# Kernel optimization log

Hardware: AMD Instinct MI355X
Metric: run time of the kernel (lower is better)

The kernel has to match this reference:

```python
import jax, jax.numpy as jnp
import numpy as np

N_NODES = 100000
N_EDGES = 1600000
NODE_IN = 64   # == node_out (residual)
EDGE_OUT = 48
HID = 128
N_GRAPHS = 64
MLP_IN = NODE_IN + 3 * EDGE_OUT + 1  # 209


def setup_inputs() -> dict:
    key = jax.random.key(0)
    ks = jax.random.split(key, 9)
    x = jax.random.normal(ks[0], (N_NODES, NODE_IN), dtype=jnp.float32)
    edge_index = jax.random.randint(ks[1], (2, N_EDGES), 0, N_NODES, dtype=jnp.int64)
    edge_attr = jax.random.normal(ks[2], (N_EDGES, EDGE_OUT), dtype=jnp.float32)
    u = jax.random.normal(ks[3], (N_GRAPHS, 1), dtype=jnp.float32)
    batch = jnp.sort(jax.random.randint(ks[4], (N_NODES,), 0, N_GRAPHS, dtype=jnp.int64))
    # MLP params (Linear stores weight [out,in]; we keep [in,out] for x @ W)
    W1 = jax.random.normal(ks[5], (MLP_IN, HID), dtype=jnp.float32) / np.sqrt(MLP_IN)
    b1 = jnp.zeros((HID,), dtype=jnp.float32)
    W2 = jax.random.normal(ks[6], (HID, NODE_IN), dtype=jnp.float32) / np.sqrt(HID)
    b2 = jnp.zeros((NODE_IN,), dtype=jnp.float32)
    return {"x": x, "edge_index": edge_index, "edge_attr": edge_attr, "u": u,
            "batch": batch, "W1": W1, "b1": b1, "W2": W2, "b2": b2}


def reference(x, edge_index, edge_attr, u, batch, W1, b1, W2, b2):
    col = edge_index[1]                      # destination node per edge
    n = x.shape[0]
    # sum / count / max over edges grouped by destination node
    s = jax.ops.segment_sum(edge_attr, col, num_segments=n)           # [N, E_out]
    cnt = jax.ops.segment_sum(jnp.ones((edge_attr.shape[0], 1), edge_attr.dtype),
                              col, num_segments=n)                    # [N, 1]
    m = jax.ops.segment_max(edge_attr, col, num_segments=n)           # [N, E_out]
    m = jnp.where(cnt > 0, m, jnp.zeros((), edge_attr.dtype))         # empty -> 0 (torch_scatter)
    mean = s / jnp.maximum(cnt, 1.0)                                  # empty -> 0
    h = jnp.concatenate([x, s, m, mean, u[batch]], axis=1)            # [N, MLP_IN]
    h = jax.nn.relu(h @ W1 + b1)
    out = h @ W2 + b2
    return out + x  # residual
```

## Files before the change

### kernel.cpp

```cpp
#include <hip/hip_runtime.h>

#define N_NODES 100000
#define N_EDGES 1600000
#define NODE_IN 64
#define EDGE_OUT 48
#define HID 128
#define MLP_IN 209
#define NB 32

__global__ void init_ws(float* __restrict__ s, float* __restrict__ m,
                        float* __restrict__ cnt) {
    int i = blockIdx.x * 256 + threadIdx.x;
    int tot = N_NODES * EDGE_OUT;
    if (i < tot) {
        s[i] = 0.0f;
        ((int*)m)[i] = 0xff800000;
    }
    if (i < N_NODES) cnt[i] = 0.0f;
}

__device__ __forceinline__ void atomicMaxF(float* addr, float val) {
    if (val >= 0.0f) {
        atomicMax((int*)addr, __float_as_int(val));
    } else {
        atomicMin((unsigned int*)addr, __float_as_uint(val));
    }
}

__global__ __launch_bounds__(256) void scatter_edges(
        const float* __restrict__ ea, const int* __restrict__ col,
        float* __restrict__ s, float* __restrict__ m, float* __restrict__ cnt) {
    int i = blockIdx.x * 256 + threadIdx.x;
    if (i >= N_EDGES * EDGE_OUT) return;
    int e = i / EDGE_OUT;
    int f = i - e * EDGE_OUT;
    float v = ea[i];
    int d = col[e];
    atomicAdd(&s[d * EDGE_OUT + f], v);
    atomicMaxF(&m[d * EDGE_OUT + f], v);
    if (f == 0) atomicAdd(&cnt[d], 1.0f);
}

__global__ __launch_bounds__(256) void mlp_kernel(
        const float* __restrict__ x, const float* __restrict__ u,
        const int* __restrict__ batch,
        const float* __restrict__ W1, const float* __restrict__ b1,
        const float* __restrict__ W2, const float* __restrict__ b2,
        const float* __restrict__ s, const float* __restrict__ m,
        const float* __restrict__ cnt, float* __restrict__ out) {
    __shared__ float h[NB][MLP_IN + 3];
    __shared__ float h1[NB][HID + 2];
    const int t = threadIdx.x;
    const int node0 = blockIdx.x * NB;

    for (int i = t; i < NB * MLP_IN; i += 256) {
        int r = i / MLP_IN;
        int c = i - r * MLP_IN;
        int g = node0 + r;
        float v;
        if (c < 64) {
            v = x[g * 64 + c];
        } else if (c < 112) {
            v = s[g * 48 + (c - 64)];
        } else if (c < 160) {
            float mv = m[g * 48 + (c - 112)];
            v = (cnt[g] > 0.0f) ? mv : 0.0f;
        } else if (c < 208) {
            v = s[g * 48 + (c - 160)] / fmaxf(cnt[g], 1.0f);
        } else {
            v = u[batch[g]];
        }
        h[r][c] = v;
    }
    __syncthreads();

    {
        const int j0 = (t & 31) * 4;
        const int r0 = (t >> 5) * 4;
        float acc[4][4];
        #pragma unroll
        for (int a = 0; a < 4; a++)
            #pragma unroll
            for (int b = 0; b < 4; b++) acc[a][b] = b1[j0 + b];
        for (int k = 0; k < MLP_IN; k++) {
            float4 w = *(const float4*)&W1[k * HID + j0];
            float hv[4];
            #pragma unroll
            for (int a = 0; a < 4; a++) hv[a] = h[r0 + a][k];
            #pragma unroll
            for (int a = 0; a < 4; a++) {
                acc[a][0] += hv[a] * w.x;
                acc[a][1] += hv[a] * w.y;
                acc[a][2] += hv[a] * w.z;
                acc[a][3] += hv[a] * w.w;
            }
        }
        #pragma unroll
        for (int a = 0; a < 4; a++)
            #pragma unroll
            for (int b = 0; b < 4; b++)
                h1[r0 + a][j0 + b] = fmaxf(acc[a][b], 0.0f);
    }
    __syncthreads();

    {
        const int j0 = (t & 15) * 4;
        const int r0 = (t >> 4) * 2;
        float acc[2][4];
        #pragma unroll
        for (int a = 0; a < 2; a++)
            #pragma unroll
            for (int b = 0; b < 4; b++) acc[a][b] = b2[j0 + b];
        for (int k = 0; k < HID; k++) {
            float4 w = *(const float4*)&W2[k * NODE_IN + j0];
            #pragma unroll
            for (int a = 0; a < 2; a++) {
                float hv = h1[r0 + a][k];
                acc[a][0] += hv * w.x;
                acc[a][1] += hv * w.y;
                acc[a][2] += hv * w.z;
                acc[a][3] += hv * w.w;
            }
        }
        #pragma unroll
        for (int a = 0; a < 2; a++) {
            int g = node0 + r0 + a;
            float4 o;
            o.x = acc[a][0] + h[r0 + a][j0 + 0];
            o.y = acc[a][1] + h[r0 + a][j0 + 1];
            o.z = acc[a][2] + h[r0 + a][j0 + 2];
            o.w = acc[a][3] + h[r0 + a][j0 + 3];
            *(float4*)&out[g * NODE_IN + j0] = o;
        }
    }
}

extern "C" void kernel_launch(void* const* d_in, const int* in_sizes, int n_in,
                              void* d_out, int out_size, void* d_ws, size_t ws_size,
                              hipStream_t stream) {
    const float* x     = (const float*)d_in[0];
    const int*   ei    = (const int*)d_in[1];
    const float* ea    = (const float*)d_in[2];
    const float* u     = (const float*)d_in[3];
    const int*   batch = (const int*)d_in[4];
    const float* W1    = (const float*)d_in[5];
    const float* b1    = (const float*)d_in[6];
    const float* W2    = (const float*)d_in[7];
    const float* b2    = (const float*)d_in[8];
    float* out = (float*)d_out;

    float* s   = (float*)d_ws;
    float* m   = s + (size_t)N_NODES * EDGE_OUT;
    float* cnt = m + (size_t)N_NODES * EDGE_OUT;

    const int* col = ei + N_EDGES;

    int initTot = N_NODES * EDGE_OUT;
    hipLaunchKernelGGL(init_ws, dim3((initTot + 255) / 256), dim3(256), 0, stream,
                       s, m, cnt);

    int scTot = N_EDGES * EDGE_OUT;
    hipLaunchKernelGGL(scatter_edges, dim3((scTot + 255) / 256), dim3(256), 0, stream,
                       ea, col, s, m, cnt);

    hipLaunchKernelGGL(mlp_kernel, dim3(N_NODES / NB), dim3(256), 0, stream,
                       x, u, batch, W1, b1, W2, b2, s, m, cnt, out);
}
```

Measured before the change: 1.315 ms.

## Replace atomic edge scatter with CSR build and fused per-node gather-reduce in MLP

Instead of scattering every edge feature with float atomicAdd and atomicMax into node-sized buffers, the edges are bucketed by destination into a CSR index (count, single-block scan, fill). The MLP kernel then gathers each node's incoming edge rows, reduces sum and max with wave shuffles, and writes the aggregates straight into a transposed shared tile. This removes about 150M atomics and the round trip of the s and m buffers through memory. In exchange it does random row gathers through eix, runs a serial single-block scan, and transposes the shared layout so the first matmul can use vectorized loads.

```diff
diff --git a/kernel.cpp b/kernel.cpp
--- a/kernel.cpp
+++ b/kernel.cpp
@@ -1,4 +1,5 @@
 #include <hip/hip_runtime.h>
+#include <math.h>
 
 #define N_NODES 100000
 #define N_EDGES 1600000
@@ -7,70 +8,122 @@
 #define HID 128
 #define MLP_IN 209
 #define NB 32
-
-__global__ void init_ws(float* __restrict__ s, float* __restrict__ m,
-                        float* __restrict__ cnt) {
+#define HTS 36
+#define H1S 132
+
+__global__ void k_zero(int* __restrict__ cur) {
     int i = blockIdx.x * 256 + threadIdx.x;
-    int tot = N_NODES * EDGE_OUT;
-    if (i < tot) {
-        s[i] = 0.0f;
-        ((int*)m)[i] = 0xff800000;
-    }
-    if (i < N_NODES) cnt[i] = 0.0f;
-}
-
-__device__ __forceinline__ void atomicMaxF(float* addr, float val) {
-    if (val >= 0.0f) {
-        atomicMax((int*)addr, __float_as_int(val));
-    } else {
-        atomicMin((unsigned int*)addr, __float_as_uint(val));
-    }
-}
-
-__global__ __launch_bounds__(256) void scatter_edges(
-        const float* __restrict__ ea, const int* __restrict__ col,
-        float* __restrict__ s, float* __restrict__ m, float* __restrict__ cnt) {
-    int i = blockIdx.x * 256 + threadIdx.x;
-    if (i >= N_EDGES * EDGE_OUT) return;
-    int e = i / EDGE_OUT;
-    int f = i - e * EDGE_OUT;
-    float v = ea[i];
-    int d = col[e];
-    atomicAdd(&s[d * EDGE_OUT + f], v);
-    atomicMaxF(&m[d * EDGE_OUT + f], v);
-    if (f == 0) atomicAdd(&cnt[d], 1.0f);
-}
-
-__global__ __launch_bounds__(256) void mlp_kernel(
-        const float* __restrict__ x, const float* __restrict__ u,
-        const int* __restrict__ batch,
+    if (i < N_NODES) cur[i] = 0;
+}
+
+__global__ __launch_bounds__(256) void k_count(const int* __restrict__ col,
+                                               int* __restrict__ cur) {
+    int e = blockIdx.x * 256 + threadIdx.x;
+    if (e < N_EDGES) atomicAdd(&cur[col[e]], 1);
+}
+
+__global__ __launch_bounds__(1024) void k_scan(int* __restrict__ cur,
+                                               int* __restrict__ off) {
+    __shared__ int part[1024];
+    const int t = threadIdx.x;
+    const int CH = (N_NODES + 1023) / 1024;
+    const int base = t * CH;
+    int sum = 0;
+    for (int i = 0; i < CH; i++) {
+        int idx = base + i;
+        if (idx < N_NODES) sum += cur[idx];
+    }
+    part[t] = sum;
+    __syncthreads();
+    for (int o = 1; o < 1024; o <<= 1) {
+        int v = 0;
+        if (t >= o) v = part[t - o];
+        __syncthreads();
+        part[t] += v;
+        __syncthreads();
+    }
+    int run = part[t] - sum;
+    for (int i = 0; i < CH; i++) {
+        int idx = base + i;
+        if (idx < N_NODES) {
+            int d = cur[idx];
+            off[idx] = run;
+            cur[idx] = run;
+            run += d;
+        }
+    }
+    if (t == 1023) off[N_NODES] = run;
+}
+
+__global__ __launch_bounds__(256) void k_fill(const int* __restrict__ col,
+                                              int* __restrict__ cur,
+                                              int* __restrict__ eix) {
+    int e = blockIdx.x * 256 + threadIdx.x;
+    if (e < N_EDGES) {
+        int pos = atomicAdd(&cur[col[e]], 1);
+        eix[pos] = e;
+    }
+}
+
+__global__ __launch_bounds__(256) void k_mlp(
+        const float* __restrict__ x, const float* __restrict__ ea,
+        const float* __restrict__ u, const int* __restrict__ batch,
         const float* __restrict__ W1, const float* __restrict__ b1,
         const float* __restrict__ W2, const float* __restrict__ b2,
-        const float* __restrict__ s, const float* __restrict__ m,
-        const float* __restrict__ cnt, float* __restrict__ out) {
-    __shared__ float h[NB][MLP_IN + 3];
-    __shared__ float h1[NB][HID + 2];
+        const int* __restrict__ off, const int* __restrict__ eix,
+        float* __restrict__ out) {
+    __shared__ float ht[MLP_IN * HTS];
+    __shared__ float h1[NB * H1S];
     const int t = threadIdx.x;
     const int node0 = blockIdx.x * NB;
 
-    for (int i = t; i < NB * MLP_IN; i += 256) {
-        int r = i / MLP_IN;
-        int c = i - r * MLP_IN;
-        int g = node0 + r;
-        float v;
-        if (c < 64) {
-            v = x[g * 64 + c];
-        } else if (c < 112) {
-            v = s[g * 48 + (c - 64)];
-        } else if (c < 160) {
-            float mv = m[g * 48 + (c - 112)];
-            v = (cnt[g] > 0.0f) ? mv : 0.0f;
-        } else if (c < 208) {
-            v = s[g * 48 + (c - 160)] / fmaxf(cnt[g], 1.0f);
-        } else {
-            v = u[batch[g]];
-        }
-        h[r][c] = v;
+    for (int i = t; i < NB * NODE_IN; i += 256) {
+        int r = i >> 6, c = i & 63;
+        ht[c * HTS + r] = x[(node0 + r) * NODE_IN + c];
+    }
+    if (t < NB) ht[208 * HTS + t] = u[batch[node0 + t]];
+
+    {
+        const int wv = t >> 6;
+        const int lane = t & 63;
+        const int f = lane & 15;
+        const int g = lane >> 4;
+        for (int i = 0; i < 8; i++) {
+            const int r = wv * 8 + i;
+            const int n = node0 + r;
+            const int beg = off[n], end = off[n + 1];
+            float s0 = 0.f, s1 = 0.f, s2 = 0.f;
+            float m0 = -INFINITY, m1 = -INFINITY, m2 = -INFINITY;
+            for (int p = beg + g; p < end; p += 4) {
+                const int e = eix[p];
+                const float* row = ea + (size_t)e * EDGE_OUT;
+                float v0 = row[f];
+                float v1 = row[f + 16];
+                float v2 = row[f + 32];
+                s0 += v0; s1 += v1; s2 += v2;
+                m0 = fmaxf(m0, v0); m1 = fmaxf(m1, v1); m2 = fmaxf(m2, v2);
+            }
+            #pragma unroll
+            for (int d = 16; d < 64; d <<= 1) {
+                s0 += __shfl_xor(s0, d); s1 += __shfl_xor(s1, d); s2 += __shfl_xor(s2, d);
+                m0 = fmaxf(m0, __shfl_xor(m0, d));
+                m1 = fmaxf(m1, __shfl_xor(m1, d));
+                m2 = fmaxf(m2, __shfl_xor(m2, d));
+            }
+            const int deg = end - beg;
+            if (lane < 16) {
+                const float fd = fmaxf((float)deg, 1.0f);
+                ht[(64 + f) * HTS + r] = s0;
+                ht[(64 + f + 16) * HTS + r] = s1;
+                ht[(64 + f + 32) * HTS + r] = s2;
+                ht[(112 + f) * HTS + r] = (deg > 0) ? m0 : 0.f;
+                ht[(112 + f + 16) * HTS + r] = (deg > 0) ? m1 : 0.f;
+                ht[(112 + f + 32) * HTS + r] = (deg > 0) ? m2 : 0.f;
+                ht[(160 + f) * HTS + r] = s0 / fd;
+                ht[(160 + f + 16) * HTS + r] = s1 / fd;
+                ht[(160 + f + 32) * HTS + r] = s2 / fd;
+            }
+        }
     }
     __syncthreads();
 
@@ -82,24 +135,20 @@
         for (int a = 0; a < 4; a++)
             #pragma unroll
             for (int b = 0; b < 4; b++) acc[a][b] = b1[j0 + b];
+        #pragma unroll 4
         for (int k = 0; k < MLP_IN; k++) {
-            float4 w = *(const float4*)&W1[k * HID + j0];
-            float hv[4];
-            #pragma unroll
-            for (int a = 0; a < 4; a++) hv[a] = h[r0 + a][k];
-            #pragma unroll
-            for (int a = 0; a < 4; a++) {
-                acc[a][0] += hv[a] * w.x;
-                acc[a][1] += hv[a] * w.y;
-                acc[a][2] += hv[a] * w.z;
-                acc[a][3] += hv[a] * w.w;
-            }
+            const float4 w = *(const float4*)&W1[k * HID + j0];
+            const float4 hv = *(const float4*)&ht[k * HTS + r0];
+            acc[0][0] += hv.x * w.x; acc[0][1] += hv.x * w.y; acc[0][2] += hv.x * w.z; acc[0][3] += hv.x * w.w;
+            acc[1][0] += hv.y * w.x; acc[1][1] += hv.y * w.y; acc[1][2] += hv.y * w.z; acc[1][3] += hv.y * w.w;
+            acc[2][0] += hv.z * w.x; acc[2][1] += hv.z * w.y; acc[2][2] += hv.z * w.z; acc[2][3] += hv.z * w.w;
+            acc[3][0] += hv.w * w.x; acc[3][1] += hv.w * w.y; acc[3][2] += hv.w * w.z; acc[3][3] += hv.w * w.w;
         }
         #pragma unroll
         for (int a = 0; a < 4; a++)
             #pragma unroll
             for (int b = 0; b < 4; b++)
-                h1[r0 + a][j0 + b] = fmaxf(acc[a][b], 0.0f);
+                h1[(r0 + a) * H1S + j0 + b] = fmaxf(acc[a][b], 0.f);
     }
     __syncthreads();
 
@@ -111,26 +160,28 @@
         for (int a = 0; a < 2; a++)
             #pragma unroll
             for (int b = 0; b < 4; b++) acc[a][b] = b2[j0 + b];
-        for (int k = 0; k < HID; k++) {
-            float4 w = *(const float4*)&W2[k * NODE_IN + j0];
-            #pragma unroll
-            for (int a = 0; a < 2; a++) {
-                float hv = h1[r0 + a][k];
-                acc[a][0] += hv * w.x;
-                acc[a][1] += hv * w.y;
-                acc[a][2] += hv * w.z;
-                acc[a][3] += hv * w.w;
+        #pragma unroll
+        for (int k4 = 0; k4 < HID; k4 += 4) {
+            float4 h0 = *(const float4*)&h1[r0 * H1S + k4];
+            float4 h1v = *(const float4*)&h1[(r0 + 1) * H1S + k4];
+            #pragma unroll
+            for (int q = 0; q < 4; q++) {
+                const float4 w = *(const float4*)&W2[(k4 + q) * NODE_IN + j0];
+                const float ha = (q == 0) ? h0.x : (q == 1) ? h0.y : (q == 2) ? h0.z : h0.w;
+                const float hb = (q == 0) ? h1v.x : (q == 1) ? h1v.y : (q == 2) ? h1v.z : h1v.w;
+                acc[0][0] += ha * w.x; acc[0][1] += ha * w.y; acc[0][2] += ha * w.z; acc[0][3] += ha * w.w;
+                acc[1][0] += hb * w.x; acc[1][1] += hb * w.y; acc[1][2] += hb * w.z; acc[1][3] += hb * w.w;
             }
         }
         #pragma unroll
         for (int a = 0; a < 2; a++) {
-            int g = node0 + r0 + a;
+            const int r = r0 + a;
             float4 o;
-            o.x = acc[a][0] + h[r0 + a][j0 + 0];
-            o.y = acc[a][1] + h[r0 + a][j0 + 1];
-            o.z = acc[a][2] + h[r0 + a][j0 + 2];
-            o.w = acc[a][3] + h[r0 + a][j0 + 3];
-            *(float4*)&out[g * NODE_IN + j0] = o;
+            o.x = acc[a][0] + ht[(j0 + 0) * HTS + r];
+            o.y = acc[a][1] + ht[(j0 + 1) * HTS + r];
+            o.z = acc[a][2] + ht[(j0 + 2) * HTS + r];
+            o.w = acc[a][3] + ht[(j0 + 3) * HTS + r];
+            *(float4*)&out[(size_t)(node0 + r) * NODE_IN + j0] = o;
         }
     }
 }
@@ -149,20 +200,16 @@
     const float* b2    = (const float*)d_in[8];
     float* out = (float*)d_out;
 
-    float* s   = (float*)d_ws;
-    float* m   = s + (size_t)N_NODES * EDGE_OUT;
-    float* cnt = m + (size_t)N_NODES * EDGE_OUT;
+    int* off = (int*)d_ws;
+    int* cur = off + (N_NODES + 1);
+    int* eix = cur + N_NODES;
 
     const int* col = ei + N_EDGES;
 
-    int initTot = N_NODES * EDGE_OUT;
-    hipLaunchKernelGGL(init_ws, dim3((initTot + 255) / 256), dim3(256), 0, stream,
-                       s, m, cnt);
-
-    int scTot = N_EDGES * EDGE_OUT;
-    hipLaunchKernelGGL(scatter_edges, dim3((scTot + 255) / 256), dim3(256), 0, stream,
-                       ea, col, s, m, cnt);
-
-    hipLaunchKernelGGL(mlp_kernel, dim3(N_NODES / NB), dim3(256), 0, stream,
-                       x, u, batch, W1, b1, W2, b2, s, m, cnt, out);
-}
+    hipLaunchKernelGGL(k_zero, dim3((N_NODES + 255) / 256), dim3(256), 0, stream, cur);
+    hipLaunchKernelGGL(k_count, dim3((N_EDGES + 255) / 256), dim3(256), 0, stream, col, cur);
+    hipLaunchKernelGGL(k_scan, dim3(1), dim3(1024), 0, stream, cur, off);
+    hipLaunchKernelGGL(k_fill, dim3((N_EDGES + 255) / 256), dim3(256), 0, stream, col, cur, eix);
+    hipLaunchKernelGGL(k_mlp, dim3(N_NODES / NB), dim3(256), 0, stream,
+                       x, ea, u, batch, W1, b1, W2, b2, off, eix, out);
+}
```

Result: faster. 1.209 ms (-8.1%).
